# Optimization experiments

Measured on AMD Instinct MI355X. Metric: run time of the kernel, lower is better.

Reference implementation:

```python
import jax, jax.numpy as jnp
import numpy as np

N = 50000       # nodes
E = 1600000     # edges (avg degree 32)
DIM = 256       # args.dim (input feature dim)
OUT = 64        # args.n_classes (output dim)
ALPHA = 0.2     # leaky relu negative slope


def setup_inputs() -> dict:
    key = jax.random.key(0)
    k1, k2, k3, k4 = jax.random.split(key, 4)
    x = jax.random.normal(k1, (N, DIM), dtype=jnp.float32)
    # sparse adjacency as COO indices: row 0 = src (output row), row 1 = dst (neighbor)
    edge_index = jax.random.randint(k2, (2, E), 0, N, dtype=jnp.int32)
    # xavier-uniform init as in SpGraphAttentionLayer
    lim_w = float(np.sqrt(6.0 / (DIM + OUT)))
    W = jax.random.uniform(k3, (DIM, OUT), minval=-lim_w, maxval=lim_w, dtype=jnp.float32)
    lim_a = float(np.sqrt(6.0 / (1 + 2 * OUT)))
    a = jax.random.uniform(k4, (2 * OUT,), minval=-lim_a, maxval=lim_a, dtype=jnp.float32)
    return {"x": x, "edge_index": edge_index, "W": W, "a": a}


def reference(x, edge_index, W, a):
    # h = x @ W : [N, OUT]
    h = x @ W
    src = edge_index[0]  # [E] output row index i
    dst = edge_index[1]  # [E] neighbor index j
    # attention logit per edge: a . concat(h[i], h[j])
    logits = h[src] @ a[:OUT] + h[dst] @ a[OUT:]          # [E]
    # edge_e = exp(-leakyrelu(logits))  (note the negation, as in SpGraphAttentionLayer)
    e = jnp.exp(-jax.nn.leaky_relu(logits, ALPHA))         # [E]
    # row-wise normalizer: sum_j e_ij
    rowsum = jax.ops.segment_sum(e, src, num_segments=N)   # [N]
    # aggregated messages: sum_j e_ij * h_j
    agg = jax.ops.segment_sum(e[:, None] * h[dst], src, num_segments=N)  # [N, OUT]
    # h' = agg / rowsum, then elu (concat=True branch)
    return jax.nn.elu(agg / rowsum[:, None])
```

## Files before the change

### kernel.cpp

```cpp
#include <hip/hip_runtime.h>

#define NN 50000
#define NE 1600000
#define DIM 256
#define OUTD 64
#define ALPHA 0.2f

#define BSH 6
#define NB ((NN + 63) >> 6)
#define CAP 3072
#define P1 128
#define EPB (NE / P1)

#define GEMM_BLOCKS ((NN + 63) / 64)
#define WSTRIDE 264

typedef unsigned short u16;
typedef unsigned int u32;
typedef __attribute__((ext_vector_type(8))) short short8;
typedef __attribute__((ext_vector_type(4))) float floatx4;

__device__ __forceinline__ u16 f2bf(float f) {
  u32 b = __float_as_uint(f);
  b += 0x7FFFu + ((b >> 16) & 1u);
  return (u16)(b >> 16);
}
__device__ __forceinline__ float bflo(u32 u) { return __uint_as_float(u << 16); }
__device__ __forceinline__ float bfhi(u32 u) { return __uint_as_float(u & 0xFFFF0000u); }

__global__ __launch_bounds__(256) void init_kernel(const float* __restrict__ W,
                                                   u32* __restrict__ wt,
                                                   int* __restrict__ bktcnt) {
  if (blockIdx.x < 4) {
    const int i = blockIdx.x * 256 + threadIdx.x;
    if (i < NB) bktcnt[i] = 0;
    return;
  }
  const int g = (blockIdx.x - 4) * 256 + threadIdx.x;
  const int n = g >> 7;
  const int kp = g & 127;
  const float lo = W[(size_t)(2 * kp) * OUTD + n];
  const float hi = W[(size_t)(2 * kp + 1) * OUTD + n];
  wt[g] = (u32)f2bf(lo) | ((u32)f2bf(hi) << 16);
}

__global__ __launch_bounds__(256) void gemm_kernel(
    const float* __restrict__ x, const u32* __restrict__ wt,
    const float* __restrict__ a, u16* __restrict__ hb,
    float* __restrict__ s1, float* __restrict__ s2)
{
  __shared__ u16 Wl[OUTD * WSTRIDE];
  const int t = threadIdx.x;
  {
    const uint4* srcv = (const uint4*)wt;
#pragma unroll
    for (int i = 0; i < 8; ++i) {
      const int c = t + 256 * i;
      const int n = c >> 5;
      const int k8 = c & 31;
      *(uint4*)&Wl[n * WSTRIDE + k8 * 8] = srcv[c];
    }
  }
  __syncthreads();

  const int lane = t & 63;
  const int wv = t >> 6;
  const int n = lane & 15;
  const int quad = lane >> 4;
  int rb = blockIdx.x * 64 + wv * 16;
  if (rb > NN - 16) rb = NN - 16;
  const int row = rb + n;
  const float4* xrow = (const float4*)(x + (size_t)row * DIM);

  floatx4 acc[4] = {{0.f, 0.f, 0.f, 0.f},
                    {0.f, 0.f, 0.f, 0.f},
                    {0.f, 0.f, 0.f, 0.f},
                    {0.f, 0.f, 0.f, 0.f}};

#pragma unroll
  for (int kk = 0; kk < 8; ++kk) {
    const float4 lo = xrow[kk * 8 + quad * 2];
    const float4 hi = xrow[kk * 8 + quad * 2 + 1];
    union { u32 u[4]; short8 s; } af;
    af.u[0] = (u32)f2bf(lo.x) | ((u32)f2bf(lo.y) << 16);
    af.u[1] = (u32)f2bf(lo.z) | ((u32)f2bf(lo.w) << 16);
    af.u[2] = (u32)f2bf(hi.x) | ((u32)f2bf(hi.y) << 16);
    af.u[3] = (u32)f2bf(hi.z) | ((u32)f2bf(hi.w) << 16);
#pragma unroll
    for (int nt = 0; nt < 4; ++nt) {
      const short8 bf =
          *(const short8*)&Wl[(nt * 16 + n) * WSTRIDE + kk * 32 + quad * 8];
      acc[nt] = __builtin_amdgcn_mfma_f32_16x16x32_bf16(af.s, bf, acc[nt], 0, 0, 0);
    }
  }

  float av1[4], av2[4];
#pragma unroll
  for (int nt = 0; nt < 4; ++nt) {
    av1[nt] = a[nt * 16 + n];
    av2[nt] = a[OUTD + nt * 16 + n];
  }

#pragma unroll
  for (int reg = 0; reg < 4; ++reg) {
    const int r = rb + quad * 4 + reg;
    float q1 = acc[0][reg] * av1[0] + acc[1][reg] * av1[1] +
               acc[2][reg] * av1[2] + acc[3][reg] * av1[3];
    float q2 = acc[0][reg] * av2[0] + acc[1][reg] * av2[1] +
               acc[2][reg] * av2[2] + acc[3][reg] * av2[3];
#pragma unroll
    for (int off = 1; off <= 8; off <<= 1) {
      q1 += __shfl_xor(q1, off);
      q2 += __shfl_xor(q2, off);
    }
    if (n == 0) { s1[r] = q1; s2[r] = q2; }
#pragma unroll
    for (int nt = 0; nt < 4; ++nt)
      hb[(size_t)r * OUTD + nt * 16 + n] = f2bf(acc[nt][reg]);
  }
}

__global__ __launch_bounds__(1024) void bin_kernel(
    const int* __restrict__ src, const int* __restrict__ dst,
    int* __restrict__ bktcnt, u32* __restrict__ binned)
{
  __shared__ int lh[NB];
  const int t = threadIdx.x;
  const int p = blockIdx.x;
  for (int i = t; i < NB; i += 1024) lh[i] = 0;
  __syncthreads();

  const int4* src4 = (const int4*)(src + p * EPB);
  const int4* dst4 = (const int4*)(dst + p * EPB);
  for (int i = t; i < EPB / 4; i += 1024) {
    const int4 s = src4[i];
    if ((u32)s.x < (u32)NN) atomicAdd(&lh[s.x >> BSH], 1);
    if ((u32)s.y < (u32)NN) atomicAdd(&lh[s.y >> BSH], 1);
    if ((u32)s.z < (u32)NN) atomicAdd(&lh[s.z >> BSH], 1);
    if ((u32)s.w < (u32)NN) atomicAdd(&lh[s.w >> BSH], 1);
  }
  __syncthreads();

  for (int b = t; b < NB; b += 1024) {
    const int c = lh[b];
    lh[b] = (c > 0) ? atomicAdd(bktcnt + b, c) + b * CAP : 0;
  }
  __syncthreads();

  for (int i = t; i < EPB / 4; i += 1024) {
    const int4 s = src4[i];
    const int4 d = dst4[i];
    int pos, b;
    if ((u32)s.x < (u32)NN) {
      b = s.x >> BSH; pos = atomicAdd(&lh[b], 1);
      if (pos < (b + 1) * CAP) binned[pos] = ((u32)(s.x & 63) << 16) | (u32)(d.x & 0xFFFF);
    }
    if ((u32)s.y < (u32)NN) {
      b = s.y >> BSH; pos = atomicAdd(&lh[b], 1);
      if (pos < (b + 1) * CAP) binned[pos] = ((u32)(s.y & 63) << 16) | (u32)(d.y & 0xFFFF);
    }
    if ((u32)s.z < (u32)NN) {
      b = s.z >> BSH; pos = atomicAdd(&lh[b], 1);
      if (pos < (b + 1) * CAP) binned[pos] = ((u32)(s.z & 63) << 16) | (u32)(d.z & 0xFFFF);
    }
    if ((u32)s.w < (u32)NN) {
      b = s.w >> BSH; pos = atomicAdd(&lh[b], 1);
      if (pos < (b + 1) * CAP) binned[pos] = ((u32)(s.w & 63) << 16) | (u32)(d.w & 0xFFFF);
    }
  }
}

__global__ __launch_bounds__(512) void bucket_agg_kernel(
    const u16* __restrict__ hb, const float* __restrict__ s1,
    const float* __restrict__ s2, const int* __restrict__ bktcnt,
    const u32* __restrict__ binned, float* __restrict__ out)
{
  __shared__ u32 ebuf[CAP];
  __shared__ u16 sdst[CAP];
  __shared__ float wls[CAP];
  __shared__ float s1l[64];
  __shared__ int cnt[64];
  __shared__ int off0[64];
  __shared__ int cur[64];
  const int b = blockIdx.x;
  const int t = threadIdx.x;
  int n = bktcnt[b];
  if (n > CAP) n = CAP;

  if (t < 64) {
    cnt[t] = 0;
    const int nd = b * 64 + t;
    s1l[t] = (nd < NN) ? s1[nd] : 0.f;
  }
  __syncthreads();

  const u32* eb = binned + (size_t)b * CAP;
  for (int i = t; i < n; i += 512) {
    const u32 v = eb[i];
    ebuf[i] = v;
    atomicAdd(&cnt[(v >> 16) & 63], 1);
  }
  __syncthreads();

  if (t < 64) {
    const int v = cnt[t];
    int xx = v;
#pragma unroll
    for (int o = 1; o < 64; o <<= 1) {
      const int y = __shfl_up(xx, o, 64);
      if (t >= o) xx += y;
    }
    off0[t] = xx - v;
    cur[t] = xx - v;
  }
  __syncthreads();

  for (int i = t; i < n; i += 512) {
    const u32 v = ebuf[i];
    const int ln = (v >> 16) & 63;
    const int d = (int)(v & 0xFFFFu);
    const int pos = atomicAdd(&cur[ln], 1);
    sdst[pos] = (u16)d;
    const float logit = s1l[ln] + s2[d];
    const float lr = logit > 0.f ? logit : ALPHA * logit;
    wls[pos] = __expf(-lr);
  }
  __syncthreads();

  const int lane = t & 63;
  const int wv = t >> 6;
  const int g = lane >> 3;
  const int seg = lane & 7;

  for (int ni = 0; ni < 8; ++ni) {
    const int ln = wv * 8 + ni;
    const int node = b * 64 + ln;
    if (node >= NN) continue;
    const int base = off0[ln];
    const int cend = base + cnt[ln];

    float a0 = 0.f, a1 = 0.f, a2 = 0.f, a3 = 0.f;
    float a4 = 0.f, a5 = 0.f, a6 = 0.f, a7 = 0.f;
    float wsum = 0.f;

    for (int e = base + g; e < cend; e += 8) {
      const int dg = sdst[e];
      const float wg = wls[e];
      const uint4 p = *(const uint4*)(hb + (size_t)dg * OUTD + seg * 8);
      a0 = fmaf(wg, bflo(p.x), a0);
      a1 = fmaf(wg, bfhi(p.x), a1);
      a2 = fmaf(wg, bflo(p.y), a2);
      a3 = fmaf(wg, bfhi(p.y), a3);
      a4 = fmaf(wg, bflo(p.z), a4);
      a5 = fmaf(wg, bfhi(p.z), a5);
      a6 = fmaf(wg, bflo(p.w), a6);
      a7 = fmaf(wg, bfhi(p.w), a7);
      wsum += wg;
    }

#pragma unroll
    for (int off = 8; off <= 32; off <<= 1) {
      a0 += __shfl_xor(a0, off);
      a1 += __shfl_xor(a1, off);
      a2 += __shfl_xor(a2, off);
      a3 += __shfl_xor(a3, off);
      a4 += __shfl_xor(a4, off);
      a5 += __shfl_xor(a5, off);
      a6 += __shfl_xor(a6, off);
      a7 += __shfl_xor(a7, off);
      wsum += __shfl_xor(wsum, off);
    }

    if (g == 0) {
      const float inv = (cnt[ln] > 0) ? 1.f / wsum : 0.f;
      float4 r;
      float v;
      v = a0 * inv; r.x = v > 0.f ? v : (__expf(v) - 1.f);
      v = a1 * inv; r.y = v > 0.f ? v : (__expf(v) - 1.f);
      v = a2 * inv; r.z = v > 0.f ? v : (__expf(v) - 1.f);
      v = a3 * inv; r.w = v > 0.f ? v : (__expf(v) - 1.f);
      *(float4*)(out + (size_t)node * OUTD + seg * 8) = r;
      v = a4 * inv; r.x = v > 0.f ? v : (__expf(v) - 1.f);
      v = a5 * inv; r.y = v > 0.f ? v : (__expf(v) - 1.f);
      v = a6 * inv; r.z = v > 0.f ? v : (__expf(v) - 1.f);
      v = a7 * inv; r.w = v > 0.f ? v : (__expf(v) - 1.f);
      *(float4*)(out + (size_t)node * OUTD + seg * 8 + 4) = r;
    }
  }
}

extern "C" void kernel_launch(void* const* d_in, const int* in_sizes, int n_in,
                              void* d_out, int out_size, void* d_ws, size_t ws_size,
                              hipStream_t stream) {
  const float* x = (const float*)d_in[0];
  const int* ei = (const int*)d_in[1];
  const float* W = (const float*)d_in[2];
  const float* a = (const float*)d_in[3];
  float* out = (float*)d_out;

  u16* hb = (u16*)d_ws;
  float* s1 = (float*)(hb + (size_t)NN * OUTD);
  float* s2 = s1 + NN;
  int* bktcnt = (int*)(s2 + NN);
  u32* wt = (u32*)(bktcnt + NB);
  u32* binned = wt + 8192;

  const int* src = ei;
  const int* dst = ei + NE;

  hipLaunchKernelGGL(init_kernel, dim3(36), dim3(256), 0, stream, W, wt, bktcnt);
  hipLaunchKernelGGL(gemm_kernel, dim3(GEMM_BLOCKS), dim3(256), 0, stream,
                     x, wt, a, hb, s1, s2);
  hipLaunchKernelGGL(bin_kernel, dim3(P1), dim3(1024), 0, stream,
                     src, dst, bktcnt, binned);
  hipLaunchKernelGGL(bucket_agg_kernel, dim3(NB), dim3(512), 0, stream,
                     hb, s1, s2, bktcnt, binned, out);
}
```

Before: 163.2 us.

## Fuse GEMM and edge binning into one launch; split aggregation buckets in half

The projection GEMM and the edge-binning pass now run as one launch with 1024-thread blocks. The first blocks compute h and the attention scores, the rest bin edges, and the binning histogram reuses the GEMM's shared-memory buffer. This removes a launch and lets the two independent stages run at the same time on the GPU. The aggregation kernel now uses two 256-thread blocks per 64-node bucket, each handling 32 nodes with smaller LDS buffers, to get more parallelism and occupancy. The cost is that each half-block reads and filters the whole bucket's edge list, and a new cap of 1792 edges per half can drop edges for unusually dense buckets.

```diff
diff --git a/kernel.cpp b/kernel.cpp
--- a/kernel.cpp
+++ b/kernel.cpp
@@ -9,10 +9,12 @@
 #define BSH 6
 #define NB ((NN + 63) >> 6)
 #define CAP 3072
+#define CAPH 1792
 #define P1 128
 #define EPB (NE / P1)
 
-#define GEMM_BLOCKS ((NN + 63) / 64)
+#define GB1024 ((NN + 255) / 256)
+#define FAT_GRID (GB1024 + P1)
 #define WSTRIDE 264
 
 typedef unsigned short u16;
@@ -44,89 +46,89 @@
   wt[g] = (u32)f2bf(lo) | ((u32)f2bf(hi) << 16);
 }
 
-__global__ __launch_bounds__(256) void gemm_kernel(
+__global__ __launch_bounds__(1024) void fat_kernel(
     const float* __restrict__ x, const u32* __restrict__ wt,
     const float* __restrict__ a, u16* __restrict__ hb,
-    float* __restrict__ s1, float* __restrict__ s2)
-{
-  __shared__ u16 Wl[OUTD * WSTRIDE];
-  const int t = threadIdx.x;
-  {
-    const uint4* srcv = (const uint4*)wt;
-#pragma unroll
-    for (int i = 0; i < 8; ++i) {
-      const int c = t + 256 * i;
-      const int n = c >> 5;
-      const int k8 = c & 31;
-      *(uint4*)&Wl[n * WSTRIDE + k8 * 8] = srcv[c];
-    }
-  }
-  __syncthreads();
-
-  const int lane = t & 63;
-  const int wv = t >> 6;
-  const int n = lane & 15;
-  const int quad = lane >> 4;
-  int rb = blockIdx.x * 64 + wv * 16;
-  if (rb > NN - 16) rb = NN - 16;
-  const int row = rb + n;
-  const float4* xrow = (const float4*)(x + (size_t)row * DIM);
-
-  floatx4 acc[4] = {{0.f, 0.f, 0.f, 0.f},
-                    {0.f, 0.f, 0.f, 0.f},
-                    {0.f, 0.f, 0.f, 0.f},
-                    {0.f, 0.f, 0.f, 0.f}};
-
-#pragma unroll
-  for (int kk = 0; kk < 8; ++kk) {
-    const float4 lo = xrow[kk * 8 + quad * 2];
-    const float4 hi = xrow[kk * 8 + quad * 2 + 1];
-    union { u32 u[4]; short8 s; } af;
-    af.u[0] = (u32)f2bf(lo.x) | ((u32)f2bf(lo.y) << 16);
-    af.u[1] = (u32)f2bf(lo.z) | ((u32)f2bf(lo.w) << 16);
-    af.u[2] = (u32)f2bf(hi.x) | ((u32)f2bf(hi.y) << 16);
-    af.u[3] = (u32)f2bf(hi.z) | ((u32)f2bf(hi.w) << 16);
-#pragma unroll
-    for (int nt = 0; nt < 4; ++nt) {
-      const short8 bf =
-          *(const short8*)&Wl[(nt * 16 + n) * WSTRIDE + kk * 32 + quad * 8];
-      acc[nt] = __builtin_amdgcn_mfma_f32_16x16x32_bf16(af.s, bf, acc[nt], 0, 0, 0);
-    }
-  }
-
-  float av1[4], av2[4];
-#pragma unroll
-  for (int nt = 0; nt < 4; ++nt) {
-    av1[nt] = a[nt * 16 + n];
-    av2[nt] = a[OUTD + nt * 16 + n];
-  }
-
-#pragma unroll
-  for (int reg = 0; reg < 4; ++reg) {
-    const int r = rb + quad * 4 + reg;
-    float q1 = acc[0][reg] * av1[0] + acc[1][reg] * av1[1] +
-               acc[2][reg] * av1[2] + acc[3][reg] * av1[3];
-    float q2 = acc[0][reg] * av2[0] + acc[1][reg] * av2[1] +
-               acc[2][reg] * av2[2] + acc[3][reg] * av2[3];
-#pragma unroll
-    for (int off = 1; off <= 8; off <<= 1) {
-      q1 += __shfl_xor(q1, off);
-      q2 += __shfl_xor(q2, off);
-    }
-    if (n == 0) { s1[r] = q1; s2[r] = q2; }
-#pragma unroll
-    for (int nt = 0; nt < 4; ++nt)
-      hb[(size_t)r * OUTD + nt * 16 + n] = f2bf(acc[nt][reg]);
-  }
-}
-
-__global__ __launch_bounds__(1024) void bin_kernel(
+    float* __restrict__ s1, float* __restrict__ s2,
     const int* __restrict__ src, const int* __restrict__ dst,
     int* __restrict__ bktcnt, u32* __restrict__ binned)
 {
-  __shared__ int lh[NB];
+  __shared__ u16 Wl[OUTD * WSTRIDE];
+  int* lh = (int*)Wl;
   const int t = threadIdx.x;
-  const int p = blockIdx.x;
+
+  if (blockIdx.x < GB1024) {
+    {
+      const uint4* srcv = (const uint4*)wt;
+#pragma unroll
+      for (int i = 0; i < 2; ++i) {
+        const int c = t + 1024 * i;
+        const int n = c >> 5;
+        const int k8 = c & 31;
+        *(uint4*)&Wl[n * WSTRIDE + k8 * 8] = srcv[c];
+      }
+    }
+    __syncthreads();
+
+    const int lane = t & 63;
+    const int wv = t >> 6;
+    const int n = lane & 15;
+    const int quad = lane >> 4;
+    int rb = blockIdx.x * 256 + wv * 16;
+    if (rb > NN - 16) rb = NN - 16;
+    const int row = rb + n;
+    const float4* xrow = (const float4*)(x + (size_t)row * DIM);
+
+    floatx4 acc[4] = {{0.f, 0.f, 0.f, 0.f},
+                      {0.f, 0.f, 0.f, 0.f},
+                      {0.f, 0.f, 0.f, 0.f},
+                      {0.f, 0.f, 0.f, 0.f}};
+
+#pragma unroll
+    for (int kk = 0; kk < 8; ++kk) {
+      const float4 lo = xrow[kk * 8 + quad * 2];
+      const float4 hi = xrow[kk * 8 + quad * 2 + 1];
+      union { u32 u[4]; short8 s; } af;
+      af.u[0] = (u32)f2bf(lo.x) | ((u32)f2bf(lo.y) << 16);
+      af.u[1] = (u32)f2bf(lo.z) | ((u32)f2bf(lo.w) << 16);
+      af.u[2] = (u32)f2bf(hi.x) | ((u32)f2bf(hi.y) << 16);
+      af.u[3] = (u32)f2bf(hi.z) | ((u32)f2bf(hi.w) << 16);
+#pragma unroll
+      for (int nt = 0; nt < 4; ++nt) {
+        const short8 bf =
+            *(const short8*)&Wl[(nt * 16 + n) * WSTRIDE + kk * 32 + quad * 8];
+        acc[nt] = __builtin_amdgcn_mfma_f32_16x16x32_bf16(af.s, bf, acc[nt], 0, 0, 0);
+      }
+    }
+
+    float av1[4], av2[4];
+#pragma unroll
+    for (int nt = 0; nt < 4; ++nt) {
+      av1[nt] = a[nt * 16 + n];
+      av2[nt] = a[OUTD + nt * 16 + n];
+    }
+
+#pragma unroll
+    for (int reg = 0; reg < 4; ++reg) {
+      const int r = rb + quad * 4 + reg;
+      float q1 = acc[0][reg] * av1[0] + acc[1][reg] * av1[1] +
+                 acc[2][reg] * av1[2] + acc[3][reg] * av1[3];
+      float q2 = acc[0][reg] * av2[0] + acc[1][reg] * av2[1] +
+                 acc[2][reg] * av2[2] + acc[3][reg] * av2[3];
+#pragma unroll
+      for (int off = 1; off <= 8; off <<= 1) {
+        q1 += __shfl_xor(q1, off);
+        q2 += __shfl_xor(q2, off);
+      }
+      if (n == 0) { s1[r] = q1; s2[r] = q2; }
+#pragma unroll
+      for (int nt = 0; nt < 4; ++nt)
+        hb[(size_t)r * OUTD + nt * 16 + n] = f2bf(acc[nt][reg]);
+    }
+    return;
+  }
+
+  const int p = blockIdx.x - GB1024;
   for (int i = t; i < NB; i += 1024) lh[i] = 0;
   __syncthreads();
 
@@ -170,44 +172,56 @@
   }
 }
 
-__global__ __launch_bounds__(512) void bucket_agg_kernel(
+__global__ __launch_bounds__(256) void bucket_agg_kernel(
     const u16* __restrict__ hb, const float* __restrict__ s1,
     const float* __restrict__ s2, const int* __restrict__ bktcnt,
     const u32* __restrict__ binned, float* __restrict__ out)
 {
-  __shared__ u32 ebuf[CAP];
-  __shared__ u16 sdst[CAP];
-  __shared__ float wls[CAP];
-  __shared__ float s1l[64];
-  __shared__ int cnt[64];
-  __shared__ int off0[64];
-  __shared__ int cur[64];
-  const int b = blockIdx.x;
+  __shared__ u32 ebuf[CAPH];
+  __shared__ u16 sdst[CAPH];
+  __shared__ float wls[CAPH];
+  __shared__ float s1l[32];
+  __shared__ int cnt[32];
+  __shared__ int off0[32];
+  __shared__ int cur[32];
+  __shared__ int ecur;
+  const int b = blockIdx.x >> 1;
+  const int sub = blockIdx.x & 1;
   const int t = threadIdx.x;
   int n = bktcnt[b];
   if (n > CAP) n = CAP;
 
-  if (t < 64) {
+  if (t < 32) {
     cnt[t] = 0;
-    const int nd = b * 64 + t;
+    const int nd = b * 64 + sub * 32 + t;
     s1l[t] = (nd < NN) ? s1[nd] : 0.f;
   }
+  if (t == 0) ecur = 0;
   __syncthreads();
 
   const u32* eb = binned + (size_t)b * CAP;
-  for (int i = t; i < n; i += 512) {
+  for (int i = t; i < n; i += 256) {
     const u32 v = eb[i];
-    ebuf[i] = v;
-    atomicAdd(&cnt[(v >> 16) & 63], 1);
-  }
-  __syncthreads();
-
-  if (t < 64) {
+    const int ln = (v >> 16) & 63;
+    if ((ln >> 5) == sub) {
+      const int pos = atomicAdd(&ecur, 1);
+      if (pos < CAPH) {
+        ebuf[pos] = v;
+        atomicAdd(&cnt[ln & 31], 1);
+      }
+    }
+  }
+  __syncthreads();
+
+  int nh = ecur;
+  if (nh > CAPH) nh = CAPH;
+
+  if (t < 32) {
     const int v = cnt[t];
     int xx = v;
 #pragma unroll
-    for (int o = 1; o < 64; o <<= 1) {
-      const int y = __shfl_up(xx, o, 64);
+    for (int o = 1; o < 32; o <<= 1) {
+      const int y = __shfl_up(xx, o, 32);
       if (t >= o) xx += y;
     }
     off0[t] = xx - v;
@@ -215,9 +229,9 @@
   }
   __syncthreads();
 
-  for (int i = t; i < n; i += 512) {
+  for (int i = t; i < nh; i += 256) {
     const u32 v = ebuf[i];
-    const int ln = (v >> 16) & 63;
+    const int ln = (v >> 16) & 31;
     const int d = (int)(v & 0xFFFFu);
     const int pos = atomicAdd(&cur[ln], 1);
     sdst[pos] = (u16)d;
@@ -234,7 +248,7 @@
 
   for (int ni = 0; ni < 8; ++ni) {
     const int ln = wv * 8 + ni;
-    const int node = b * 64 + ln;
+    const int node = b * 64 + sub * 32 + ln;
     if (node >= NN) continue;
     const int base = off0[ln];
     const int cend = base + cnt[ln];
@@ -309,10 +323,8 @@
   const int* dst = ei + NE;
 
   hipLaunchKernelGGL(init_kernel, dim3(36), dim3(256), 0, stream, W, wt, bktcnt);
-  hipLaunchKernelGGL(gemm_kernel, dim3(GEMM_BLOCKS), dim3(256), 0, stream,
-                     x, wt, a, hb, s1, s2);
-  hipLaunchKernelGGL(bin_kernel, dim3(P1), dim3(1024), 0, stream,
-                     src, dst, bktcnt, binned);
-  hipLaunchKernelGGL(bucket_agg_kernel, dim3(NB), dim3(512), 0, stream,
+  hipLaunchKernelGGL(fat_kernel, dim3(FAT_GRID), dim3(1024), 0, stream,
+                     x, wt, a, hb, s1, s2, src, dst, bktcnt, binned);
+  hipLaunchKernelGGL(bucket_agg_kernel, dim3(2 * NB), dim3(256), 0, stream,
                      hb, s1, s2, bktcnt, binned, out);
 }
```

After: 156.7 us. 4.0% less time.
